# Optimization experiments

Hardware: AMD Instinct MI355X
Metric: run time of the kernel (lower is better)

## Reference

```python
import jax, jax.numpy as jnp
import numpy as np

HIDDEN = 4096
N_HEADS = 32
N_KV_HEADS = 8
HEAD_SIZE = HIDDEN // N_HEADS  # 128
ROPE_THETA = 10000.0
SEQ_LEN = 1024
BATCH = 4


def setup_inputs() -> dict:
    key = jax.random.key(0)
    k1, k2, k3 = jax.random.split(key, 3)
    scale = 1.0 / np.sqrt(HIDDEN)
    hidden_states = jax.random.normal(k1, (BATCH * SEQ_LEN, HIDDEN), dtype=jnp.float32)
    w_qkv = jax.random.normal(k2, ((N_HEADS + 2 * N_KV_HEADS) * HEAD_SIZE, HIDDEN), dtype=jnp.float32) * scale
    w_o = jax.random.normal(k3, (HIDDEN, N_HEADS * HEAD_SIZE), dtype=jnp.float32) * scale
    return {"hidden_states": hidden_states, "w_qkv": w_qkv, "w_o": w_o, "seq_len": SEQ_LEN}


def _rope(x, pos, theta):
    # x: [B, S, H, D]; pos: [S] absolute positions; rotate-half (LLAMA/NeoX) style
    d = x.shape[-1]
    inv_freq = 1.0 / (theta ** (jnp.arange(0, d, 2, dtype=jnp.float32) / d))  # [D/2]
    ang = pos.astype(jnp.float32)[:, None] * inv_freq[None, :]  # [S, D/2]
    cos = jnp.cos(ang)[None, :, None, :]
    sin = jnp.sin(ang)[None, :, None, :]
    x1, x2 = jnp.split(x, 2, axis=-1)
    return jnp.concatenate([x1 * cos - x2 * sin, x2 * cos + x1 * sin], axis=-1)


def reference(hidden_states, w_qkv, w_o, seq_len):
    total, hidden = hidden_states.shape
    B = total // seq_len
    hd = HEAD_SIZE
    # fused QKV projection (bias-free), split like the torch module
    qkv = hidden_states @ w_qkv.T  # [T, (H+2K)*hd]
    q, k, v = jnp.split(qkv, [N_HEADS * hd, (N_HEADS + N_KV_HEADS) * hd], axis=1)
    q = q.reshape(B, seq_len, N_HEADS, hd)
    k = k.reshape(B, seq_len, N_KV_HEADS, hd)
    v = v.reshape(B, seq_len, N_KV_HEADS, hd)
    # inline RoPE (ROPE_LLAMA) on q and k at absolute positions
    pos = jnp.arange(seq_len)
    q = _rope(q, pos, ROPE_THETA)
    k = _rope(k, pos, ROPE_THETA)
    # GQA: map each q head to its kv head (kv_head_mapping = repeat_interleave)
    groups = N_HEADS // N_KV_HEADS
    k = jnp.repeat(k, groups, axis=2)  # [B, S, H, hd]
    v = jnp.repeat(v, groups, axis=2)
    scale = hd ** -0.5
    scores = jnp.einsum('bqhd,bkhd->bhqk', q, k) * scale  # [B, H, S, S]
    causal = jnp.tril(jnp.ones((seq_len, seq_len), dtype=bool))
    scores = jnp.where(causal[None, None], scores, jnp.finfo(scores.dtype).min)
    probs = jax.nn.softmax(scores, axis=-1)
    attn = jnp.einsum('bhqk,bkhd->bqhd', probs, v).reshape(total, N_HEADS * hd)
    return attn @ w_o.T  # [T, hidden]
```

## Files before the change

kernel.cpp:

```cpp
#include <hip/hip_runtime.h>


typedef short bf16x8 __attribute__((ext_vector_type(8)));
typedef short bf16x4 __attribute__((ext_vector_type(4)));
typedef float floatx4 __attribute__((ext_vector_type(4)));
typedef unsigned short u16x8 __attribute__((ext_vector_type(8)));

__device__ __forceinline__ unsigned short f2bf(float f) {
  unsigned u = __float_as_uint(f);
  u += 0x7FFFu + ((u >> 16) & 1u);
  return (unsigned short)(u >> 16);
}
__device__ __forceinline__ float bf2f(unsigned short h) {
  return __uint_as_float(((unsigned)h) << 16);
}

__device__ __forceinline__ void async16(const void* g, void* l) {
  __builtin_amdgcn_global_load_lds(
      (const __attribute__((address_space(1))) unsigned int*)g,
      (__attribute__((address_space(3))) unsigned int*)l, 16, 0, 0);
}

__global__ void cvt_xw(const float4* __restrict__ X,
                       const float4* __restrict__ Wq,
                       u16x8* __restrict__ Xb, u16x8* __restrict__ Wqb) {
  const float4* src;
  u16x8* dst;
  int i;
  if (blockIdx.x < 8192) {
    src = X; dst = Xb; i = blockIdx.x * 256 + threadIdx.x;
  } else {
    src = Wq; dst = Wqb; i = (blockIdx.x - 8192) * 256 + threadIdx.x;
  }
  float4 a = src[2 * i], b = src[2 * i + 1];
  u16x8 o;
  o[0] = f2bf(a.x); o[1] = f2bf(a.y); o[2] = f2bf(a.z); o[3] = f2bf(a.w);
  o[4] = f2bf(b.x); o[5] = f2bf(b.y); o[6] = f2bf(b.z); o[7] = f2bf(b.w);
  dst[i] = o;
}

__global__ void cvt_f32_bf16(const float4* __restrict__ in,
                             u16x8* __restrict__ out, int n8) {
  int i = blockIdx.x * 256 + threadIdx.x;
  if (i < n8) {
    float4 a = in[2 * i], b = in[2 * i + 1];
    u16x8 o;
    o[0] = f2bf(a.x); o[1] = f2bf(a.y); o[2] = f2bf(a.z); o[3] = f2bf(a.w);
    o[4] = f2bf(b.x); o[5] = f2bf(b.y); o[6] = f2bf(b.z); o[7] = f2bf(b.w);
    out[i] = o;
  }
}

template <int OUT_BF16>
__global__ __launch_bounds__(512, 2) void gemm256(
    const unsigned short* __restrict__ A, const unsigned short* __restrict__ B,
    void* __restrict__ Cout, int M, int N, int K) {
  __shared__ __align__(16) unsigned short As[4][8192];
  __shared__ __align__(16) unsigned short Bs[4][8192];
  const int tid = threadIdx.x;
  const int wave = tid >> 6, lane = tid & 63;
  const int wm = wave >> 2, wn = wave & 3;
  const int l16 = lane & 15, c4 = lane >> 4;
  const int bm = blockIdx.y << 8, bn = blockIdx.x << 8;

  int afOff[8], bfOff[4];
#pragma unroll
  for (int mi = 0; mi < 8; ++mi) {
    int r = wm * 128 + mi * 16 + l16;
    int pr = r >> 1, l8 = ((r & 1) << 2) | c4;
    afOff[mi] = pr * 128 + ((l8 ^ (pr & 7)) << 4);
  }
#pragma unroll
  for (int ni = 0; ni < 4; ++ni) {
    int r = wn * 64 + ni * 16 + l16;
    int pr = r >> 1, l8 = ((r & 1) << 2) | c4;
    bfOff[ni] = pr * 128 + ((l8 ^ (pr & 7)) << 4);
  }

  const int sp = lane >> 3;
  const int l8s = (lane & 7) ^ sp;
  const int so = l8s >> 2, sc = (l8s & 3) << 3;
  const unsigned short* aS0 = A + (size_t)(bm + wave * 16 + sp * 2 + so) * K + sc;
  const unsigned short* aS1 = A + (size_t)(bm + (wave + 8) * 16 + sp * 2 + so) * K + sc;
  const unsigned short* bS0 = B + (size_t)(bn + wave * 16 + sp * 2 + so) * K + sc;
  const unsigned short* bS1 = B + (size_t)(bn + (wave + 8) * 16 + sp * 2 + so) * K + sc;
  const int dst0 = wave * 1024, dst1 = (wave + 8) * 1024;

  floatx4 acc[8][4];
#pragma unroll
  for (int mi = 0; mi < 8; ++mi)
#pragma unroll
    for (int ni = 0; ni < 4; ++ni) acc[mi][ni] = (floatx4){0.f, 0.f, 0.f, 0.f};

  const int NT = K >> 5;
  async16(aS0, (char*)As[0] + dst0);
  async16(aS1, (char*)As[0] + dst1);
  async16(bS0, (char*)Bs[0] + dst0);
  async16(bS1, (char*)Bs[0] + dst1);
  async16(aS0 + 32, (char*)As[1] + dst0);
  async16(aS1 + 32, (char*)As[1] + dst1);
  async16(bS0 + 32, (char*)Bs[1] + dst0);
  async16(bS1 + 32, (char*)Bs[1] + dst1);
  asm volatile("s_waitcnt vmcnt(4)" ::: "memory");
  __builtin_amdgcn_s_barrier();

  bf16x8 afq0[4], afq1[4], bfcA[4], bfcB[4];
#pragma unroll
  for (int i = 0; i < 4; ++i)
    afq0[i] = *(const bf16x8*)((const char*)As[0] + afOff[i]);
#pragma unroll
  for (int i = 0; i < 4; ++i)
    bfcA[i] = *(const bf16x8*)((const char*)Bs[0] + bfOff[i]);

  size_t koff = 64;

#define KTILE(T, BC, BN_)                                                     \
  {                                                                           \
    const char* aB = (const char*)As[(T) & 3];                                \
    const char* aN = (const char*)As[((T) + 1) & 3];                          \
    const char* bN = (const char*)Bs[((T) + 1) & 3];                          \
    char* aD = (char*)As[((T) + 2) & 3];                                      \
    char* bD = (char*)Bs[((T) + 2) & 3];                                      \
    _Pragma("unroll") for (int i = 0; i < 4; ++i)                             \
        afq1[i] = *(const bf16x8*)(aB + afOff[4 + i]);                        \
    async16(aS0 + koff, aD + dst0);                                           \
    async16(aS1 + koff, aD + dst1);                                           \
    __builtin_amdgcn_s_barrier();                                             \
    __builtin_amdgcn_s_setprio(1);                                            \
    _Pragma("unroll") for (int mi = 0; mi < 4; ++mi)                          \
        _Pragma("unroll") for (int ni = 0; ni < 4; ++ni)                      \
            acc[mi][ni] = __builtin_amdgcn_mfma_f32_16x16x32_bf16(            \
                afq0[mi], BC[ni], acc[mi][ni], 0, 0, 0);                      \
    __builtin_amdgcn_s_setprio(0);                                            \
    asm volatile("s_waitcnt vmcnt(2)" ::: "memory");   \
    __builtin_amdgcn_s_barrier();                     \
    _Pragma("unroll") for (int i = 0; i < 4; ++i)                             \
        afq0[i] = *(const bf16x8*)(aN + afOff[i]);                            \
    _Pragma("unroll") for (int i = 0; i < 4; ++i)                             \
        BN_[i] = *(const bf16x8*)(bN + bfOff[i]);                             \
    async16(bS0 + koff, bD + dst0);                                           \
    async16(bS1 + koff, bD + dst1);                                           \
    __builtin_amdgcn_s_barrier();                                             \
    __builtin_amdgcn_s_setprio(1);                                            \
    _Pragma("unroll") for (int mi = 0; mi < 4; ++mi)                          \
        _Pragma("unroll") for (int ni = 0; ni < 4; ++ni)                      \
            acc[4 + mi][ni] = __builtin_amdgcn_mfma_f32_16x16x32_bf16(        \
                afq1[mi], BC[ni], acc[4 + mi][ni], 0, 0, 0);                  \
    __builtin_amdgcn_s_setprio(0);                                            \
    __builtin_amdgcn_s_barrier();                                             \
    koff += 32;                                                               \
  }

  for (int t = 0; t < NT; t += 2) {
    KTILE(t, bfcA, bfcB);
    KTILE(t + 1, bfcB, bfcA);
  }
#undef KTILE

  const int col0 = bn + wn * 64 + l16;
#pragma unroll
  for (int mi = 0; mi < 8; ++mi) {
    const int row0 = bm + wm * 128 + mi * 16 + c4 * 4;
#pragma unroll
    for (int ni = 0; ni < 4; ++ni)
#pragma unroll
      for (int r = 0; r < 4; ++r) {
        if (OUT_BF16)
          ((unsigned short*)Cout)[(size_t)(row0 + r) * N + col0 + ni * 16] =
              f2bf(acc[mi][ni][r]);
        else
          ((float*)Cout)[(size_t)(row0 + r) * N + col0 + ni * 16] =
              acc[mi][ni][r];
      }
  }
}

__global__ void rope_k_kernel(unsigned short* __restrict__ qkv) {
  const int t = blockIdx.x;
  const int s = t & 1023;
  const int head = 32 + blockIdx.y * 4 + (threadIdx.x >> 6);
  const int d = threadIdx.x & 63;
  unsigned short* p = qkv + (size_t)t * 6144 + head * 128;
  float x1 = bf2f(p[d]), x2 = bf2f(p[d + 64]);
  float inv_freq = exp2f((float)d * -0.20762050593046015f);
  float ang = (float)s * inv_freq;
  float c, sn;
  __sincosf(ang, &sn, &c);
  p[d] = f2bf(x1 * c - x2 * sn);
  p[d + 64] = f2bf(x2 * c + x1 * sn);
}

__device__ __constant__ int QTS[6][3] = {
    {15, 4, 3}, {14, 5, 2}, {13, 6, 1}, {12, 7, 0}, {11, 8, -1}, {10, 9, -1}};

__global__ __launch_bounds__(256, 3) void flash_attn(
    const unsigned short* __restrict__ qkv, unsigned short* __restrict__ aout) {
  const int pr = blockIdx.x;
  const int h = blockIdx.y, b = blockIdx.z;
  const int kh = h >> 2;
  const int tid = threadIdx.x;
  const int wave = tid >> 6, lane = tid & 63;
  const int quad = lane >> 4, l16 = lane & 15;

  __shared__ __align__(16) unsigned short Ks[64][136];
  __shared__ __align__(16) unsigned short Vt[128][68];
  __shared__ __align__(16) unsigned short Ps[64][68];

  const int krow = tid >> 4, kcol = (tid & 15) << 3;
  const int vrb = (tid & 15) << 2, vcol = (tid >> 4) << 3;
  const unsigned short* kp = qkv + (size_t)(b << 10) * 6144 + 4096 + kh * 128;
  const unsigned short* vp = qkv + (size_t)(b << 10) * 6144 + 5120 + kh * 128;

  for (int qi = 0; qi < 3; ++qi) {
    const int qt = QTS[pr][qi];
    if (qt < 0) break;
    const int q0 = qt << 6;

    bf16x8 qf[4];
    {
      const int qrow = q0 + wave * 16 + l16;
      const unsigned short* qp =
          qkv + (size_t)((b << 10) + qrow) * 6144 + h * 128 + quad * 8;
#pragma unroll
      for (int ks = 0; ks < 4; ++ks) qf[ks] = *(const bf16x8*)(qp + ks * 32);
      const float pos = (float)qrow;
      const float scale = 0.08838834764831845f;
#pragma unroll
      for (int ks = 0; ks < 2; ++ks)
#pragma unroll
        for (int e = 0; e < 8; ++e) {
          int d = ks * 32 + quad * 8 + e;
          float ang = pos * exp2f((float)d * -0.20762050593046015f);
          float c, sn;
          __sincosf(ang, &sn, &c);
          float x1 = bf2f((unsigned short)qf[ks][e]);
          float x2 = bf2f((unsigned short)qf[ks + 2][e]);
          qf[ks][e] = (short)f2bf((x1 * c - x2 * sn) * scale);
          qf[ks + 2][e] = (short)f2bf((x2 * c + x1 * sn) * scale);
        }
    }

    floatx4 o_acc[8];
#pragma unroll
    for (int i = 0; i < 8; ++i) o_acc[i] = (floatx4){0.f, 0.f, 0.f, 0.f};
    float l_lane[4] = {0.f, 0.f, 0.f, 0.f};

    bf16x8 kreg[4], vreg[4];
#pragma unroll
    for (int j = 0; j < 4; ++j)
      kreg[j] = *(const bf16x8*)(kp + (size_t)(krow + j * 16) * 6144 + kcol);
#pragma unroll
    for (int j = 0; j < 4; ++j)
      vreg[j] = *(const bf16x8*)(vp + (size_t)(vrb + j) * 6144 + vcol);

    for (int t = 0; t <= qt; ++t) {
      __syncthreads();
#pragma unroll
      for (int j = 0; j < 4; ++j)
        *(bf16x8*)&Ks[krow + j * 16][kcol] = kreg[j];
#pragma unroll
      for (int e = 0; e < 8; ++e) {
        bf16x4 w = {vreg[0][e], vreg[1][e], vreg[2][e], vreg[3][e]};
        *(bf16x4*)&Vt[vcol + e][vrb] = w;
      }
      __syncthreads();
      if (t < qt) {
        const size_t nb = (size_t)((t + 1) << 6) * 6144;
#pragma unroll
        for (int j = 0; j < 4; ++j)
          kreg[j] =
              *(const bf16x8*)(kp + nb + (size_t)(krow + j * 16) * 6144 + kcol);
#pragma unroll
        for (int j = 0; j < 4; ++j)
          vreg[j] = *(const bf16x8*)(vp + nb + (size_t)(vrb + j) * 6144 + vcol);
      }

      floatx4 sacc[4];
#pragma unroll
      for (int ni = 0; ni < 4; ++ni) sacc[ni] = (floatx4){0.f, 0.f, 0.f, 0.f};
#pragma unroll
      for (int ks = 0; ks < 4; ++ks)
#pragma unroll
        for (int ni = 0; ni < 4; ++ni) {
          bf16x8 kf = *(const bf16x8*)&Ks[ni * 16 + l16][ks * 32 + quad * 8];
          sacc[ni] = __builtin_amdgcn_mfma_f32_16x16x32_bf16(qf[ks], kf,
                                                             sacc[ni], 0, 0, 0);
        }

      const bool masked = (t == qt);
#pragma unroll
      for (int r = 0; r < 4; ++r) {
        float rs = 0.f;
#pragma unroll
        for (int ni = 0; ni < 4; ++ni) {
          float e = __expf(sacc[ni][r]);
          if (masked && (ni * 16 + l16) > (wave * 16 + quad * 4 + r)) e = 0.f;
          rs += e;
          Ps[wave * 16 + quad * 4 + r][ni * 16 + l16] = f2bf(e);
        }
        l_lane[r] += rs;
      }
      asm volatile("s_waitcnt lgkmcnt(0)" ::: "memory");

#pragma unroll
      for (int ks2 = 0; ks2 < 2; ++ks2) {
        bf16x8 pf = *(const bf16x8*)&Ps[wave * 16 + l16][ks2 * 32 + quad * 8];
#pragma unroll
        for (int n8 = 0; n8 < 8; ++n8) {
          bf16x8 vf = *(const bf16x8*)&Vt[n8 * 16 + l16][ks2 * 32 + quad * 8];
          o_acc[n8] = __builtin_amdgcn_mfma_f32_16x16x32_bf16(pf, vf, o_acc[n8],
                                                              0, 0, 0);
        }
      }
    }

#pragma unroll
    for (int r = 0; r < 4; ++r) {
      float l = l_lane[r];
#pragma unroll
      for (int off = 1; off < 16; off <<= 1) l += __shfl_xor(l, off, 64);
      float inv = 1.0f / l;
      int row = q0 + wave * 16 + quad * 4 + r;
      unsigned short* op = aout + (size_t)((b << 10) + row) * 4096 + h * 128;
#pragma unroll
      for (int n8 = 0; n8 < 8; ++n8)
        op[n8 * 16 + l16] = f2bf(o_acc[n8][r] * inv);
    }
  }
}

extern "C" void kernel_launch(void* const* d_in, const int* in_sizes, int n_in,
                              void* d_out, int out_size, void* d_ws,
                              size_t ws_size, hipStream_t stream) {
  const float* X = (const float*)d_in[0];
  const float* Wqkv = (const float*)d_in[1];
  const float* Wo = (const float*)d_in[2];
  (void)in_sizes; (void)n_in; (void)out_size; (void)ws_size;

  char* ws = (char*)d_ws;
  unsigned short* Wqkvb = (unsigned short*)ws;
  unsigned short* AttnB = (unsigned short*)ws;
  unsigned short* Xb = (unsigned short*)(ws + 50331648);
  unsigned short* Wob = (unsigned short*)(ws + 50331648);
  unsigned short* QKVb = (unsigned short*)(ws + 83886080);

  cvt_xw<<<20480, 256, 0, stream>>>((const float4*)X, (const float4*)Wqkv,
                                    (u16x8*)Xb, (u16x8*)Wqkvb);
  gemm256<1><<<dim3(24, 16), 512, 0, stream>>>(Xb, Wqkvb, QKVb, 4096, 6144, 4096);
  rope_k_kernel<<<dim3(4096, 2), 256, 0, stream>>>(QKVb);
  cvt_f32_bf16<<<8192, 256, 0, stream>>>((const float4*)Wo, (u16x8*)Wob, 2097152);
  flash_attn<<<dim3(6, 32, 4), 256, 0, stream>>>(QKVb, AttnB);
  gemm256<0><<<dim3(16, 16), 512, 0, stream>>>(AttnB, Wob, d_out, 4096, 4096, 4096);
}
```

Measured before the change: 658.4 us.

## Use 256x384 tiles for QKV GEMM and pair causal q-tiles in attention

Adds a gemm384 kernel with 256x384 output tiles and triple-buffered LDS for the QKV projection. The grid becomes 16x16 = 256 blocks, one per CU, instead of 384 blocks of 256x256, which removes the partial second wave. Flash attention now gives each block two q-tiles (15-pr and pr), so the causal work per block is equal across 8x32x4 blocks, replacing the earlier 6-block table of uneven groupings. The larger tile raises register and LDS use and limits occupancy to one block per CU.

```diff
diff --git a/kernel.cpp b/kernel.cpp
--- a/kernel.cpp
+++ b/kernel.cpp
@@ -48,6 +48,137 @@
     o[0] = f2bf(a.x); o[1] = f2bf(a.y); o[2] = f2bf(a.z); o[3] = f2bf(a.w);
     o[4] = f2bf(b.x); o[5] = f2bf(b.y); o[6] = f2bf(b.z); o[7] = f2bf(b.w);
     out[i] = o;
+  }
+}
+
+__global__ __launch_bounds__(512, 1) void gemm384(
+    const unsigned short* __restrict__ A, const unsigned short* __restrict__ B,
+    unsigned short* __restrict__ Cout, int M, int N, int K) {
+  __shared__ __align__(16) unsigned short As[3][8192];
+  __shared__ __align__(16) unsigned short Bs[3][12288];
+  const int tid = threadIdx.x;
+  const int wave = tid >> 6, lane = tid & 63;
+  const int wm = wave >> 2, wn = wave & 3;
+  const int l16 = lane & 15, c4 = lane >> 4;
+  const int bm = blockIdx.y << 8, bn = blockIdx.x * 384;
+
+  int afOff[8], bfOff[6];
+#pragma unroll
+  for (int mi = 0; mi < 8; ++mi) {
+    int r = wm * 128 + mi * 16 + l16;
+    int pr = r >> 1, l8 = ((r & 1) << 2) | c4;
+    afOff[mi] = pr * 128 + ((l8 ^ (pr & 7)) << 4);
+  }
+#pragma unroll
+  for (int ni = 0; ni < 6; ++ni) {
+    int r = wn * 96 + ni * 16 + l16;
+    int pr = r >> 1, l8 = ((r & 1) << 2) | c4;
+    bfOff[ni] = pr * 128 + ((l8 ^ (pr & 7)) << 4);
+  }
+
+  const int sp = lane >> 3;
+  const int l8s = (lane & 7) ^ sp;
+  const int so = l8s >> 2, sc = (l8s & 3) << 3;
+  const unsigned short* aS0 = A + (size_t)(bm + wave * 16 + sp * 2 + so) * K + sc;
+  const unsigned short* aS1 = A + (size_t)(bm + (wave + 8) * 16 + sp * 2 + so) * K + sc;
+  const unsigned short* bS0 = B + (size_t)(bn + (wave * 3 + 0) * 16 + sp * 2 + so) * K + sc;
+  const unsigned short* bS1 = B + (size_t)(bn + (wave * 3 + 1) * 16 + sp * 2 + so) * K + sc;
+  const unsigned short* bS2 = B + (size_t)(bn + (wave * 3 + 2) * 16 + sp * 2 + so) * K + sc;
+  const int dA0 = wave * 1024, dA1 = (wave + 8) * 1024;
+  const int dB0 = wave * 3072, dB1 = dB0 + 1024, dB2 = dB0 + 2048;
+
+  floatx4 acc[8][6];
+#pragma unroll
+  for (int mi = 0; mi < 8; ++mi)
+#pragma unroll
+    for (int ni = 0; ni < 6; ++ni) acc[mi][ni] = (floatx4){0.f, 0.f, 0.f, 0.f};
+
+  const int NT = K >> 5;
+  async16(aS0, (char*)As[0] + dA0);
+  async16(aS1, (char*)As[0] + dA1);
+  async16(bS0, (char*)Bs[0] + dB0);
+  async16(bS1, (char*)Bs[0] + dB1);
+  async16(bS2, (char*)Bs[0] + dB2);
+  async16(aS0 + 32, (char*)As[1] + dA0);
+  async16(aS1 + 32, (char*)As[1] + dA1);
+  async16(bS0 + 32, (char*)Bs[1] + dB0);
+  async16(bS1 + 32, (char*)Bs[1] + dB1);
+  async16(bS2 + 32, (char*)Bs[1] + dB2);
+  asm volatile("s_waitcnt vmcnt(5)" ::: "memory");
+  __builtin_amdgcn_s_barrier();
+
+  bf16x8 afq0[4], afq1[4], bfc[6];
+#pragma unroll
+  for (int i = 0; i < 4; ++i)
+    afq0[i] = *(const bf16x8*)((const char*)As[0] + afOff[i]);
+#pragma unroll
+  for (int i = 0; i < 6; ++i)
+    bfc[i] = *(const bf16x8*)((const char*)Bs[0] + bfOff[i]);
+
+  const char* aCur = (const char*)As[0];
+  const char* aNxt = (const char*)As[1];
+  const char* aStg = (const char*)As[2];
+  const char* bCur = (const char*)Bs[0];
+  const char* bNxt = (const char*)Bs[1];
+  const char* bStg = (const char*)Bs[2];
+
+  size_t koff = 64;
+#pragma unroll 2
+  for (int t = 0; t < NT; ++t) {
+#pragma unroll
+    for (int i = 0; i < 4; ++i)
+      afq1[i] = *(const bf16x8*)(aCur + afOff[4 + i]);
+    async16(aS0 + koff, (char*)aStg + dA0);
+    async16(aS1 + koff, (char*)aStg + dA1);
+    __builtin_amdgcn_s_barrier();
+    __builtin_amdgcn_s_setprio(1);
+#pragma unroll
+    for (int mi = 0; mi < 4; ++mi)
+#pragma unroll
+      for (int ni = 0; ni < 6; ++ni)
+        acc[mi][ni] = __builtin_amdgcn_mfma_f32_16x16x32_bf16(
+            afq0[mi], bfc[ni], acc[mi][ni], 0, 0, 0);
+    __builtin_amdgcn_s_setprio(0);
+    asm volatile("s_waitcnt vmcnt(2)" ::: "memory");
+    __builtin_amdgcn_s_barrier();
+
+    bf16x8 bfn[6];
+#pragma unroll
+    for (int i = 0; i < 4; ++i)
+      afq0[i] = *(const bf16x8*)(aNxt + afOff[i]);
+#pragma unroll
+    for (int i = 0; i < 6; ++i)
+      bfn[i] = *(const bf16x8*)(bNxt + bfOff[i]);
+    async16(bS0 + koff, (char*)bStg + dB0);
+    async16(bS1 + koff, (char*)bStg + dB1);
+    async16(bS2 + koff, (char*)bStg + dB2);
+    __builtin_amdgcn_s_barrier();
+    __builtin_amdgcn_s_setprio(1);
+#pragma unroll
+    for (int mi = 0; mi < 4; ++mi)
+#pragma unroll
+      for (int ni = 0; ni < 6; ++ni)
+        acc[4 + mi][ni] = __builtin_amdgcn_mfma_f32_16x16x32_bf16(
+            afq1[mi], bfc[ni], acc[4 + mi][ni], 0, 0, 0);
+    __builtin_amdgcn_s_setprio(0);
+    __builtin_amdgcn_s_barrier();
+#pragma unroll
+    for (int i = 0; i < 6; ++i) bfc[i] = bfn[i];
+    const char* ta = aCur; aCur = aNxt; aNxt = aStg; aStg = ta;
+    const char* tb = bCur; bCur = bNxt; bNxt = bStg; bStg = tb;
+    koff += 32;
+  }
+  (void)bCur;
+
+  const int col0 = bn + wn * 96 + l16;
+#pragma unroll
+  for (int mi = 0; mi < 8; ++mi) {
+    const int row0 = bm + wm * 128 + mi * 16 + c4 * 4;
+#pragma unroll
+    for (int ni = 0; ni < 6; ++ni)
+#pragma unroll
+      for (int r = 0; r < 4; ++r)
+        Cout[(size_t)(row0 + r) * N + col0 + ni * 16] = f2bf(acc[mi][ni][r]);
   }
 }
 
@@ -190,9 +321,6 @@
   p[d + 64] = f2bf(x2 * c + x1 * sn);
 }
 
-__device__ __constant__ int QTS[6][3] = {
-    {15, 4, 3}, {14, 5, 2}, {13, 6, 1}, {12, 7, 0}, {11, 8, -1}, {10, 9, -1}};
-
 __global__ __launch_bounds__(256, 3) void flash_attn(
     const unsigned short* __restrict__ qkv, unsigned short* __restrict__ aout) {
   const int pr = blockIdx.x;
@@ -211,9 +339,8 @@
   const unsigned short* kp = qkv + (size_t)(b << 10) * 6144 + 4096 + kh * 128;
   const unsigned short* vp = qkv + (size_t)(b << 10) * 6144 + 5120 + kh * 128;
 
-  for (int qi = 0; qi < 3; ++qi) {
-    const int qt = QTS[pr][qi];
-    if (qt < 0) break;
+  for (int half = 0; half < 2; ++half) {
+    const int qt = half ? pr : 15 - pr;
     const int q0 = qt << 6;
 
     bf16x8 qf[4];
@@ -346,9 +473,9 @@
 
   cvt_xw<<<20480, 256, 0, stream>>>((const float4*)X, (const float4*)Wqkv,
                                     (u16x8*)Xb, (u16x8*)Wqkvb);
-  gemm256<1><<<dim3(24, 16), 512, 0, stream>>>(Xb, Wqkvb, QKVb, 4096, 6144, 4096);
+  gemm384<<<dim3(16, 16), 512, 0, stream>>>(Xb, Wqkvb, QKVb, 4096, 6144, 4096);
   rope_k_kernel<<<dim3(4096, 2), 256, 0, stream>>>(QKVb);
   cvt_f32_bf16<<<8192, 256, 0, stream>>>((const float4*)Wo, (u16x8*)Wob, 2097152);
-  flash_attn<<<dim3(6, 32, 4), 256, 0, stream>>>(QKVb, AttnB);
+  flash_attn<<<dim3(8, 32, 4), 256, 0, stream>>>(QKVb, AttnB);
   gemm256<0><<<dim3(16, 16), 512, 0, stream>>>(AttnB, Wob, d_out, 4096, 4096, 4096);
 }
```

Result: slower. 1.457 ms (+121.3%).
